# Kernel tuning notes

Measured on AMD Instinct MI355X. Metric: run time of the kernel, lower is better.

## Reference

```python
import jax, jax.numpy as jnp
import numpy as np

B, QL, ML = 8, 128, 1024
QS, KS, H = 512, 512, 256


def setup_inputs() -> dict:
    key = jax.random.key(0)
    ks = jax.random.split(key, 10)
    query = jax.random.normal(ks[0], (B, QL, QS), dtype=jnp.float32)
    memory = jax.random.normal(ks[1], (B, ML, KS), dtype=jnp.float32)
    mask = jax.random.bernoulli(ks[2], 0.1, (B, ML))
    mask = mask.at[:, 0].set(False)  # ensure at least one valid position per row
    s_q = 1.0 / np.sqrt(QS)
    s_k = 1.0 / np.sqrt(KS)
    s_h = 1.0 / np.sqrt(H)
    Wq = jax.random.uniform(ks[3], (H, QS), jnp.float32, -s_q, s_q)
    bq = jax.random.uniform(ks[4], (H,), jnp.float32, -s_q, s_q)
    Wk = jax.random.uniform(ks[5], (H, KS), jnp.float32, -s_k, s_k)
    bk = jax.random.uniform(ks[6], (H,), jnp.float32, -s_k, s_k)
    wl = jax.random.uniform(ks[7], (H,), jnp.float32, -s_h, s_h)
    bl = jax.random.uniform(ks[8], (), jnp.float32, -s_h, s_h)
    return {"query": query, "memory": memory, "mask": mask,
            "Wq": Wq, "bq": bq, "Wk": Wk, "bk": bk, "wl": wl, "bl": bl}


def reference(query, memory, mask, Wq, bq, Wk, bk, wl, bl):
    # q: [B, QL, H], k: [B, ML, H]
    q = jnp.einsum('bqs,hs->bqh', query, Wq) + bq
    k = jnp.einsum('bms,hs->bmh', memory, Wk) + bk
    # additive score: tanh(q + k) projected to scalar  -> [B, QL, ML]
    z = jnp.tanh(q[:, :, None, :] + k[:, None, :, :])  # [B, QL, ML, H]
    logits = jnp.einsum('bqmh,h->bqm', z, wl) + bl
    logits = jnp.where(mask[:, None, :], jnp.float32(-1e18), logits)
    weights = jax.nn.softmax(logits, axis=-1)  # BottleSoftmax over mem_len
    attns = jnp.einsum('bqm,bms->bqs', weights, memory)
    return attns, weights
```

## Files before the change

### kernel.cpp

```cpp
#include <hip/hip_runtime.h>

#define B_  8
#define QL_ 128
#define ML_ 1024
#define KS_ 512
#define H_  256

#define QP_OFF 0
#define KP_OFF 262144
#define MASK_OFF 2359296
#define WH_OFF 2361344
#define WL_OFF 2492416
#define MT_H_OFF 2623488
#define MT_L_OFF 4720640
#define WB_H_OFF 6817792
#define WB_L_OFF 7342080
#define XH_OFF 7866368
#define XL_OFF 10225664
#define WLP_OFF 12584960

typedef __attribute__((ext_vector_type(8))) short bfrag;
typedef __attribute__((ext_vector_type(4))) float f4acc;
typedef __attribute__((ext_vector_type(2))) float f2;

__device__ __forceinline__ void split1(float v, unsigned& h, unsigned& lo) {
    unsigned u  = __float_as_uint(v);
    unsigned hb = u & 0xFFFF0000u;
    float    lf = v - __uint_as_float(hb);
    unsigned ul = __float_as_uint(lf);
    unsigned lr = ul + 0x7FFFu + ((ul >> 16) & 1u);
    h  = u >> 16;
    lo = lr >> 16;
}

__device__ __forceinline__ void split4(const float4& a, unsigned& h01, unsigned& h23,
                                       unsigned& l01, unsigned& l23) {
    unsigned h[4], l[4];
    split1(a.x, h[0], l[0]); split1(a.y, h[1], l[1]);
    split1(a.z, h[2], l[2]); split1(a.w, h[3], l[3]);
    h01 = h[0] | (h[1] << 16); h23 = h[2] | (h[3] << 16);
    l01 = l[0] | (l[1] << 16); l23 = l[2] | (l[3] << 16);
}

__global__ __launch_bounds__(256) void prep_kernel(
    const float* __restrict__ query, const float* __restrict__ memory,
    const float* __restrict__ Wq, const float* __restrict__ Wk,
    const float* __restrict__ wl,
    unsigned short* __restrict__ Whi, unsigned short* __restrict__ Wlo,
    unsigned short* __restrict__ Xhi, unsigned short* __restrict__ Xlo,
    unsigned short* __restrict__ MThi, unsigned short* __restrict__ MTlo,
    const unsigned char* __restrict__ mraw, unsigned char* __restrict__ mout,
    float* __restrict__ wlp) {
    const int bid = blockIdx.x;
    const int t = threadIdx.x;

    if (bid == 2240) {
        wlp[(t & ~7) | (((t & 3) << 1) | ((t >> 2) & 1))] = wl[t];
        __shared__ int s_not01, s_not0f;
        const unsigned int* w = (const unsigned int*)mraw;
        if (t == 0) { s_not01 = 0; s_not0f = 0; }
        __syncthreads();
        int not01 = 0, not0f = 0;
        for (int i = t; i < 2048; i += 256) {
            unsigned int v = w[i];
            if (v != 0u && v != 1u) not01 = 1;
            if (v != 0u && v != 0x3F800000u) not0f = 1;
        }
        if (not01) atomicOr(&s_not01, 1);
        if (not0f) atomicOr(&s_not0f, 1);
        __syncthreads();
        int wordTyped = (!s_not01) || (!s_not0f);
        for (int i = t; i < B_ * ML_; i += 256) {
            unsigned char mv;
            if (wordTyped) mv = (w[i] != 0u) ? 1 : 0;
            else           mv = mraw[i] ? 1 : 0;
            mout[i] = mv;
        }
        return;
    }

    if (bid >= 1216) {
        const int idx = bid - 1216;
        const int b  = idx >> 7;
        const int r  = idx & 127;
        const int mt = r >> 3;
        const int st = r & 7;
        __shared__ float T[64][68];

        const int i  = t >> 2, jb = (t & 3) << 4;
        const float* mp = memory + ((size_t)(b * ML_ + mt * 64 + i)) * KS_ + st * 64 + jb;
#pragma unroll
        for (int q = 0; q < 4; ++q)
            *(float4*)(&T[i][jb + q * 4]) = *(const float4*)(mp + q * 4);
        __syncthreads();

        const int s = t >> 2, mb = (t & 3) << 4;
        unsigned hh[16], ll[16];
#pragma unroll
        for (int e = 0; e < 16; ++e) split1(T[mb + e][s], hh[e], ll[e]);
        unsigned hp[8], lp[8];
#pragma unroll
        for (int e = 0; e < 8; ++e) {
            hp[e] = hh[2 * e] | (hh[2 * e + 1] << 16);
            lp[e] = ll[2 * e] | (ll[2 * e + 1] << 16);
        }
        const size_t doff = ((size_t)(b * KS_ + st * 64 + s)) * ML_ + mt * 64 + mb;
        *(uint4*)(MThi + doff)     = make_uint4(hp[0], hp[1], hp[2], hp[3]);
        *(uint4*)(MThi + doff + 8) = make_uint4(hp[4], hp[5], hp[6], hp[7]);
        *(uint4*)(MTlo + doff)     = make_uint4(lp[0], lp[1], lp[2], lp[3]);
        *(uint4*)(MTlo + doff + 8) = make_uint4(lp[4], lp[5], lp[6], lp[7]);
        return;
    }

    const float* src; unsigned short *dh, *dl; size_t soff, doff;
    if (bid < 64) {
        src = (bid < 32) ? Wq : Wk;
        soff = (size_t)(bid & 31) * 4096;
        doff = ((bid < 32) ? 0 : 131072) + soff;
        dh = Whi; dl = Wlo;
    } else if (bid < 192) {
        src = query;  soff = (size_t)(bid - 64) * 4096;  doff = soff;
        dh = Xhi; dl = Xlo;
    } else {
        src = memory; soff = (size_t)(bid - 192) * 4096; doff = 524288 + soff;
        dh = Xhi; dl = Xlo;
    }
    soff += (size_t)t * 16; doff += (size_t)t * 16;

    unsigned hw[8], lw[8];
#pragma unroll
    for (int i = 0; i < 4; ++i) {
        float4 v = *(const float4*)(src + soff + i * 4);
        split4(v, hw[i * 2], hw[i * 2 + 1], lw[i * 2], lw[i * 2 + 1]);
    }
    *(uint4*)(dh + doff)     = make_uint4(hw[0], hw[1], hw[2], hw[3]);
    *(uint4*)(dh + doff + 8) = make_uint4(hw[4], hw[5], hw[6], hw[7]);
    *(uint4*)(dl + doff)     = make_uint4(lw[0], lw[1], lw[2], lw[3]);
    *(uint4*)(dl + doff + 8) = make_uint4(lw[4], lw[5], lw[6], lw[7]);
}

__global__ __launch_bounds__(256) void proj_kernel(
    const unsigned short* __restrict__ Xhi, const unsigned short* __restrict__ Xlo,
    const unsigned short* __restrict__ Whi, const unsigned short* __restrict__ Wlo,
    const float* __restrict__ bq, const float* __restrict__ bk,
    float* __restrict__ Eq, float* __restrict__ Ek) {
    const int bid = blockIdx.x;
    const int t = threadIdx.x;
    const int wk = (bid & 7) * 144 + (bid >> 3);
    const int nt = wk & 3;
    const int mt = wk >> 2;

    const bool isQ = (mt < 32);
    const int arow0 = mt * 32;
    const int orow0 = isQ ? arow0 : arow0 - 1024;
    const float* bias = isQ ? bq : bk;
    float* out = isQ ? Eq : Ek;
    const int wrb = (isQ ? 0 : 256) + nt * 64;

    const int w  = t >> 6;
    const int wm = w >> 1, wn = w & 1;
    const int l  = t & 63;
    const int lr = l & 15, lk = l >> 4;

    __shared__ unsigned short As[2][2][32][64];
    __shared__ unsigned short Bs[2][2][64][64];

    const int pa   = t >> 7;
    const int slot = t & 127;
    const int arow = slot >> 2, ao = slot & 3;
    const int brow = slot >> 1, bo0 = (slot & 1) * 4;
    const unsigned short* asrc = (pa ? Xlo : Xhi) + (size_t)(arow0 + arow) * 512 + ao * 8;
    const unsigned short* bsrc = (pa ? Wlo : Whi) + (size_t)(wrb + brow) * 512 + bo0 * 8;
    const int awd0 = (ao ^ (arow & 7)) * 8;
    const int awd1 = ((ao + 4) ^ (arow & 7)) * 8;
    int bwd[4];
#pragma unroll
    for (int i = 0; i < 4; ++i) bwd[i] = ((bo0 + i) ^ (brow & 7)) * 8;

    f4acc acc[2];
    acc[0] = (f4acc){0.f, 0.f, 0.f, 0.f};
    acc[1] = (f4acc){0.f, 0.f, 0.f, 0.f};

    uint4 g0a0, g0a1, g0b0, g0b1, g0b2, g0b3;
    uint4 g1a0, g1a1, g1b0, g1b1, g1b2, g1b3;

#define LOADG(G, c) do {                                                  \
    G##a0 = *(const uint4*)(asrc + (size_t)(c) * 64);                     \
    G##a1 = *(const uint4*)(asrc + (size_t)(c) * 64 + 32);                \
    G##b0 = *(const uint4*)(bsrc + (size_t)(c) * 64);                     \
    G##b1 = *(const uint4*)(bsrc + (size_t)(c) * 64 + 8);                 \
    G##b2 = *(const uint4*)(bsrc + (size_t)(c) * 64 + 16);                \
    G##b3 = *(const uint4*)(bsrc + (size_t)(c) * 64 + 24); } while (0)

#define WRITEB(P, G) do {                                                 \
    *(uint4*)(&As[P][pa][arow][awd0])  = G##a0;                           \
    *(uint4*)(&As[P][pa][arow][awd1])  = G##a1;                           \
    *(uint4*)(&Bs[P][pa][brow][bwd[0]]) = G##b0;                          \
    *(uint4*)(&Bs[P][pa][brow][bwd[1]]) = G##b1;                          \
    *(uint4*)(&Bs[P][pa][brow][bwd[2]]) = G##b2;                          \
    *(uint4*)(&Bs[P][pa][brow][bwd[3]]) = G##b3; } while (0)

#define COMPUTE(P) do {                                                   \
    _Pragma("unroll")                                                     \
    for (int ks = 0; ks < 2; ++ks) {                                      \
        const int ra = wm * 16 + lr;                                      \
        const int koA = ((ks * 4 + lk) ^ (ra & 7)) * 8;                   \
        bfrag ah = *(const bfrag*)&As[P][0][ra][koA];                     \
        bfrag al = *(const bfrag*)&As[P][1][ra][koA];                     \
        _Pragma("unroll")                                                 \
        for (int ni = 0; ni < 2; ++ni) {                                  \
            const int rb = wn * 32 + ni * 16 + lr;                        \
            const int koB = ((ks * 4 + lk) ^ (rb & 7)) * 8;               \
            bfrag bh = *(const bfrag*)&Bs[P][0][rb][koB];                 \
            bfrag bl = *(const bfrag*)&Bs[P][1][rb][koB];                 \
            acc[ni] = __builtin_amdgcn_mfma_f32_16x16x32_bf16(            \
                ah, bh, acc[ni], 0, 0, 0);                                \
            acc[ni] = __builtin_amdgcn_mfma_f32_16x16x32_bf16(            \
                ah, bl, acc[ni], 0, 0, 0);                                \
            acc[ni] = __builtin_amdgcn_mfma_f32_16x16x32_bf16(            \
                al, bh, acc[ni], 0, 0, 0);                                \
        }                                                                 \
    } } while (0)

    LOADG(g0, 0);
    WRITEB(0, g0);
    LOADG(g1, 1);
    __syncthreads();

#pragma unroll
    for (int c = 0; c < 8; ++c) {
        if (c + 1 < 8) {
            if ((c + 1) & 1) WRITEB(1, g1); else WRITEB(0, g0);
        }
        if (c + 2 < 8) {
            if (c & 1) LOADG(g1, c + 2); else LOADG(g0, c + 2);
        }
        COMPUTE(c & 1);
        __syncthreads();
    }
#undef LOADG
#undef WRITEB
#undef COMPUTE

    const float SC = 2.885390081777926815f;
#pragma unroll
    for (int ni = 0; ni < 2; ++ni) {
        const int col = nt * 64 + wn * 32 + ni * 16 + lr;
        const int colp = (col & ~7) | (((col & 3) << 1) | ((col >> 2) & 1));
        const float bc = bias[col];
#pragma unroll
        for (int rr = 0; rr < 4; ++rr) {
            const int row = orow0 + wm * 16 + lk * 4 + rr;
            out[(size_t)row * 256 + colp] =
                __builtin_amdgcn_exp2f(SC * (acc[ni][rr] + bc));
        }
    }
}

__device__ __forceinline__ f2 qterm8(const float4 k4a, const float4 k4b,
                                     const float4 q4a, const float4 q4b,
                                     const float4 w4a, const float4 w4b,
                                     f2 acc) {
    f2 kp0 = {k4a.x, k4a.y}, kp1 = {k4a.z, k4a.w};
    f2 kp2 = {k4b.x, k4b.y}, kp3 = {k4b.z, k4b.w};
    f2 qp0 = {q4a.x, q4a.y}, qp1 = {q4a.z, q4a.w};
    f2 qp2 = {q4b.x, q4b.y}, qp3 = {q4b.z, q4b.w};
    f2 wp0 = {w4a.x, w4a.y}, wp1 = {w4a.z, w4a.w};
    f2 wp2 = {w4b.x, w4b.y}, wp3 = {w4b.z, w4b.w};
    const f2 one2 = {1.0f, 1.0f};
    f2 pp0 = __builtin_elementwise_fma(kp0, qp0, one2);
    f2 pp1 = __builtin_elementwise_fma(kp1, qp1, one2);
    f2 pp2 = __builtin_elementwise_fma(kp2, qp2, one2);
    f2 pp3 = __builtin_elementwise_fma(kp3, qp3, one2);
    f2 p01 = pp0 * pp1, p23 = pp2 * pp3;
    f2 n01 = __builtin_elementwise_fma(wp1, pp0, wp0 * pp1);
    f2 n23 = __builtin_elementwise_fma(wp3, pp2, wp2 * pp3);
    f2 Nm  = __builtin_elementwise_fma(n23, p01, n01 * p23);
    f2 P   = p01 * p23;
    f2 r   = {__builtin_amdgcn_rcpf(P.x), __builtin_amdgcn_rcpf(P.y)};
    return __builtin_elementwise_fma(Nm, r, acc);
}

__global__ __launch_bounds__(256) void logits_kernel(
    const float* __restrict__ Eq, const float* __restrict__ Ek,
    const float* __restrict__ wlp, float* __restrict__ sr) {
    const int bid = blockIdx.x;
    const int b  = bid & 7;
    const int r2 = bid >> 3;
    const int mt = r2 & 7;
    const int qt = r2 >> 3;
    const int tid = threadIdx.x;
    const int m  = tid & 127;
    const int qh = __builtin_amdgcn_readfirstlane(tid >> 7);

    __shared__ float kq[2][4][128][4];

    const float* qpb = Eq + ((size_t)(b * QL_ + qt * 8 + qh * 4)) * H_;
    const float* kpb = Ek + ((size_t)(b * ML_ + mt * 128)) * H_;

    const int srow = tid & 127;
    const int sq2  = tid >> 7;
    const float* kst = kpb + (size_t)srow * H_ + 8 * sq2;

    float4 a0 = *(const float4*)(kst);
    float4 a1 = *(const float4*)(kst + 4);
    *(float4*)(&kq[0][2 * sq2 + 0][srow][0]) = a0;
    *(float4*)(&kq[0][2 * sq2 + 1][srow][0]) = a1;
    a0 = *(const float4*)(kst + 16);
    a1 = *(const float4*)(kst + 20);
    __syncthreads();

    f2 accp[4];
#pragma unroll
    for (int j2 = 0; j2 < 4; ++j2) accp[j2] = (f2){0.f, 0.f};

    for (int c = 0; c < 16; ++c) {
        const int cb = c & 1;
        if (c < 15) {
            *(float4*)(&kq[cb ^ 1][2 * sq2 + 0][srow][0]) = a0;
            *(float4*)(&kq[cb ^ 1][2 * sq2 + 1][srow][0]) = a1;
            if (c < 14) {
                a0 = *(const float4*)(kst + (c + 2) * 16);
                a1 = *(const float4*)(kst + (c + 2) * 16 + 4);
            }
        }
        const int h0 = c * 16;
#pragma unroll
        for (int pg = 0; pg < 2; ++pg) {
            float4 k4a = *(const float4*)(&kq[cb][2 * pg + 0][m][0]);
            float4 k4b = *(const float4*)(&kq[cb][2 * pg + 1][m][0]);
            float4 w4a = *(const float4*)(wlp + h0 + pg * 8);
            float4 w4b = *(const float4*)(wlp + h0 + pg * 8 + 4);
#pragma unroll
            for (int j2 = 0; j2 < 4; ++j2) {
                float4 q4a = *(const float4*)(qpb + (size_t)j2 * H_ + h0 + pg * 8);
                float4 q4b = *(const float4*)(qpb + (size_t)j2 * H_ + h0 + pg * 8 + 4);
                accp[j2] = qterm8(k4a, k4b, q4a, q4b, w4a, w4b, accp[j2]);
            }
        }
        __syncthreads();
    }
#pragma unroll
    for (int j2 = 0; j2 < 4; ++j2)
        sr[((size_t)(b * QL_ + qt * 8 + qh * 4 + j2)) * ML_ + mt * 128 + m] =
            accp[j2].x + accp[j2].y;
}

__global__ __launch_bounds__(256) void softmax_kernel(
    float* __restrict__ wrow_io, const unsigned char* __restrict__ mv,
    unsigned short* __restrict__ Wbhi, unsigned short* __restrict__ Wblo) {
    const int row = blockIdx.x;
    const int b = row >> 7;
    const int tid = threadIdx.x;
    float* srow = wrow_io + (size_t)row * ML_;
    const unsigned char* mrow = mv + b * ML_;
    __shared__ float red[4];

    float4 s4 = *(const float4*)(srow + tid * 4);
    uchar4 m4 = *(const uchar4*)(mrow + tid * 4);
    float l[4];
    l[0] = m4.x ? -1e18f : -2.0f * s4.x;
    l[1] = m4.y ? -1e18f : -2.0f * s4.y;
    l[2] = m4.z ? -1e18f : -2.0f * s4.z;
    l[3] = m4.w ? -1e18f : -2.0f * s4.w;

    float mx = fmaxf(fmaxf(l[0], l[1]), fmaxf(l[2], l[3]));
#pragma unroll
    for (int off = 32; off >= 1; off >>= 1)
        mx = fmaxf(mx, __shfl_xor(mx, off));
    if ((tid & 63) == 0) red[tid >> 6] = mx;
    __syncthreads();
    mx = fmaxf(fmaxf(red[0], red[1]), fmaxf(red[2], red[3]));
    __syncthreads();

    const float L2E = 1.44269504088896340736f;
    float e[4], s = 0.f;
#pragma unroll
    for (int i = 0; i < 4; ++i) {
        e[i] = __builtin_amdgcn_exp2f((l[i] - mx) * L2E);
        s += e[i];
    }
#pragma unroll
    for (int off = 32; off >= 1; off >>= 1)
        s += __shfl_xor(s, off);
    if ((tid & 63) == 0) red[tid >> 6] = s;
    __syncthreads();
    s = (red[0] + red[1]) + (red[2] + red[3]);
    float inv = __builtin_amdgcn_rcpf(s);
    float4 o = make_float4(e[0] * inv, e[1] * inv, e[2] * inv, e[3] * inv);
    *(float4*)(srow + tid * 4) = o;

    unsigned h01, h23, l01, l23;
    split4(o, h01, h23, l01, l23);
    *(uint2*)(Wbhi + (size_t)row * ML_ + tid * 4) = make_uint2(h01, h23);
    *(uint2*)(Wblo + (size_t)row * ML_ + tid * 4) = make_uint2(l01, l23);
}

__global__ __launch_bounds__(256) void attn_out_kernel(
    const unsigned short* __restrict__ Wbhi, const unsigned short* __restrict__ Wblo,
    const unsigned short* __restrict__ MThi, const unsigned short* __restrict__ MTlo,
    float* __restrict__ out) {
    const int bid = blockIdx.x;
    const int b  = bid & 7;
    const int r  = bid >> 3;
    const int mt = r & 7;
    const int nt = r >> 3;
    const int t = threadIdx.x;
    const int w  = t >> 6;
    const int l  = t & 63;
    const int lr = l & 15, lk = l >> 4;

    __shared__ unsigned short As[2][16][2][64];
    __shared__ unsigned short Bs[2][64][2][64];

    const int pa  = t >> 7;
    const int ar  = (t >> 3) & 15;
    const int acq = t & 7;
    const unsigned short* asrc = (pa ? Wblo : Wbhi)
        + ((size_t)(b * QL_ + mt * 16 + ar)) * ML_ + acq * 8;
    const int aws = (acq ^ (ar & 7)) * 8;

    const int pb  = t >> 7;
    const int br  = (t & 127) >> 1;
    const int bq0 = (t & 1) * 4;
    const unsigned short* bsrc = (pb ? MTlo : MThi)
        + ((size_t)(b * KS_ + nt * 64 + br)) * ML_ + bq0 * 8;
    int bws[4];
#pragma unroll
    for (int i2 = 0; i2 < 4; ++i2) bws[i2] = ((bq0 + i2) ^ (br & 7)) * 8;

    f4acc acc = (f4acc){0.f, 0.f, 0.f, 0.f};

    uint4 g0a, g0b0, g0b1, g0b2, g0b3;
    uint4 g1a, g1b0, g1b1, g1b2, g1b3;

#define LOADG(G, c) do {                                                  \
    G##a  = *(const uint4*)(asrc + (size_t)(c) * 64);                     \
    G##b0 = *(const uint4*)(bsrc + (size_t)(c) * 64);                     \
    G##b1 = *(const uint4*)(bsrc + (size_t)(c) * 64 + 8);                 \
    G##b2 = *(const uint4*)(bsrc + (size_t)(c) * 64 + 16);                \
    G##b3 = *(const uint4*)(bsrc + (size_t)(c) * 64 + 24); } while (0)

#define WRITEB(P, G) do {                                                 \
    *(uint4*)(&As[P][ar][pa][aws])    = G##a;                             \
    *(uint4*)(&Bs[P][br][pb][bws[0]]) = G##b0;                            \
    *(uint4*)(&Bs[P][br][pb][bws[1]]) = G##b1;                            \
    *(uint4*)(&Bs[P][br][pb][bws[2]]) = G##b2;                            \
    *(uint4*)(&Bs[P][br][pb][bws[3]]) = G##b3; } while (0)

#define COMPUTE(P) do {                                                   \
    _Pragma("unroll")                                                     \
    for (int ks = 0; ks < 2; ++ks) {                                      \
        const int k8 = (ks * 4 + lk) ^ (lr & 7);                          \
        bfrag ah = *(const bfrag*)&As[P][lr][0][k8 * 8];                  \
        bfrag al = *(const bfrag*)&As[P][lr][1][k8 * 8];                  \
        bfrag bh = *(const bfrag*)&Bs[P][w * 16 + lr][0][k8 * 8];         \
        bfrag bl = *(const bfrag*)&Bs[P][w * 16 + lr][1][k8 * 8];         \
        acc = __builtin_amdgcn_mfma_f32_16x16x32_bf16(ah, bh, acc, 0,0,0);\
        acc = __builtin_amdgcn_mfma_f32_16x16x32_bf16(ah, bl, acc, 0,0,0);\
        acc = __builtin_amdgcn_mfma_f32_16x16x32_bf16(al, bh, acc, 0,0,0);\
    } } while (0)

    LOADG(g0, 0);
    WRITEB(0, g0);
    LOADG(g1, 1);
    __syncthreads();

#pragma unroll
    for (int c = 0; c < 16; ++c) {
        if (c + 1 < 16) {
            if ((c + 1) & 1) WRITEB(1, g1); else WRITEB(0, g0);
        }
        if (c + 2 < 16) {
            if (c & 1) LOADG(g1, c + 2); else LOADG(g0, c + 2);
        }
        COMPUTE(c & 1);
        __syncthreads();
    }
#undef LOADG
#undef WRITEB
#undef COMPUTE

    const int col = nt * 64 + w * 16 + lr;
#pragma unroll
    for (int rr = 0; rr < 4; ++rr) {
        const int row = mt * 16 + lk * 4 + rr;
        out[((size_t)(b * QL_ + row)) * KS_ + col] = acc[rr];
    }
}

extern "C" void kernel_launch(void* const* d_in, const int* in_sizes, int n_in,
                              void* d_out, int out_size, void* d_ws, size_t ws_size,
                              hipStream_t stream) {
    const float* query  = (const float*)d_in[0];
    const float* memory = (const float*)d_in[1];
    const unsigned char* mask = (const unsigned char*)d_in[2];
    const float* Wq = (const float*)d_in[3];
    const float* bq = (const float*)d_in[4];
    const float* Wk = (const float*)d_in[5];
    const float* bk = (const float*)d_in[6];
    const float* wl = (const float*)d_in[7];

    float* ws = (float*)d_ws;
    float* Eq = ws + QP_OFF;
    float* Ek = ws + KP_OFF;
    unsigned char* mcan = (unsigned char*)(ws + MASK_OFF);
    unsigned short* Whi  = (unsigned short*)(ws + WH_OFF);
    unsigned short* Wlo  = (unsigned short*)(ws + WL_OFF);
    unsigned short* MThi = (unsigned short*)(ws + MT_H_OFF);
    unsigned short* MTlo = (unsigned short*)(ws + MT_L_OFF);
    unsigned short* Wbhi = (unsigned short*)(ws + WB_H_OFF);
    unsigned short* Wblo = (unsigned short*)(ws + WB_L_OFF);
    unsigned short* Xhi  = (unsigned short*)(ws + XH_OFF);
    unsigned short* Xlo  = (unsigned short*)(ws + XL_OFF);
    float* wlp = ws + WLP_OFF;

    float* attns = (float*)d_out;
    float* wout  = (float*)d_out + B_ * QL_ * KS_;

    prep_kernel<<<dim3(2241), dim3(256), 0, stream>>>(query, memory, Wq, Wk, wl,
                                                      Whi, Wlo, Xhi, Xlo,
                                                      MThi, MTlo, mask, mcan, wlp);
    proj_kernel<<<dim3(1152), dim3(256), 0, stream>>>(Xhi, Xlo, Whi, Wlo,
                                                      bq, bk, Eq, Ek);
    logits_kernel<<<dim3(1024), dim3(256), 0, stream>>>(Eq, Ek, wlp, wout);
    softmax_kernel<<<dim3(B_ * QL_), dim3(256), 0, stream>>>(wout, mcan, Wbhi, Wblo);
    attn_out_kernel<<<dim3(512), dim3(256), 0, stream>>>(Wbhi, Wblo, MThi, MTlo, attns);
}
```

Baseline: 156.9 us.

## Move memory transpose-split into softmax launch and retile logits kernel

Result: no change. 158.5 us (+1.0%).

```diff
diff --git a/kernel.cpp b/kernel.cpp
--- a/kernel.cpp
+++ b/kernel.cpp
@@ -48,13 +48,12 @@
     const float* __restrict__ wl,
     unsigned short* __restrict__ Whi, unsigned short* __restrict__ Wlo,
     unsigned short* __restrict__ Xhi, unsigned short* __restrict__ Xlo,
-    unsigned short* __restrict__ MThi, unsigned short* __restrict__ MTlo,
     const unsigned char* __restrict__ mraw, unsigned char* __restrict__ mout,
     float* __restrict__ wlp) {
     const int bid = blockIdx.x;
     const int t = threadIdx.x;
 
-    if (bid == 2240) {
+    if (bid == 1216) {
         wlp[(t & ~7) | (((t & 3) << 1) | ((t >> 2) & 1))] = wl[t];
         __shared__ int s_not01, s_not0f;
         const unsigned int* w = (const unsigned int*)mraw;
@@ -76,39 +75,6 @@
             else           mv = mraw[i] ? 1 : 0;
             mout[i] = mv;
         }
-        return;
-    }
-
-    if (bid >= 1216) {
-        const int idx = bid - 1216;
-        const int b  = idx >> 7;
-        const int r  = idx & 127;
-        const int mt = r >> 3;
-        const int st = r & 7;
-        __shared__ float T[64][68];
-
-        const int i  = t >> 2, jb = (t & 3) << 4;
-        const float* mp = memory + ((size_t)(b * ML_ + mt * 64 + i)) * KS_ + st * 64 + jb;
-#pragma unroll
-        for (int q = 0; q < 4; ++q)
-            *(float4*)(&T[i][jb + q * 4]) = *(const float4*)(mp + q * 4);
-        __syncthreads();
-
-        const int s = t >> 2, mb = (t & 3) << 4;
-        unsigned hh[16], ll[16];
-#pragma unroll
-        for (int e = 0; e < 16; ++e) split1(T[mb + e][s], hh[e], ll[e]);
-        unsigned hp[8], lp[8];
-#pragma unroll
-        for (int e = 0; e < 8; ++e) {
-            hp[e] = hh[2 * e] | (hh[2 * e + 1] << 16);
-            lp[e] = ll[2 * e] | (ll[2 * e + 1] << 16);
-        }
-        const size_t doff = ((size_t)(b * KS_ + st * 64 + s)) * ML_ + mt * 64 + mb;
-        *(uint4*)(MThi + doff)     = make_uint4(hp[0], hp[1], hp[2], hp[3]);
-        *(uint4*)(MThi + doff + 8) = make_uint4(hp[4], hp[5], hp[6], hp[7]);
-        *(uint4*)(MTlo + doff)     = make_uint4(lp[0], lp[1], lp[2], lp[3]);
-        *(uint4*)(MTlo + doff + 8) = make_uint4(lp[4], lp[5], lp[6], lp[7]);
         return;
     }
 
@@ -287,71 +253,107 @@
     const int bid = blockIdx.x;
     const int b  = bid & 7;
     const int r2 = bid >> 3;
-    const int mt = r2 & 7;
-    const int qt = r2 >> 3;
+    const int mt = r2 & 15;
+    const int qt = r2 >> 4;
     const int tid = threadIdx.x;
-    const int m  = tid & 127;
-    const int qh = __builtin_amdgcn_readfirstlane(tid >> 7);
-
-    __shared__ float kq[2][4][128][4];
-
-    const float* qpb = Eq + ((size_t)(b * QL_ + qt * 8 + qh * 4)) * H_;
-    const float* kpb = Ek + ((size_t)(b * ML_ + mt * 128)) * H_;
-
-    const int srow = tid & 127;
-    const int sq2  = tid >> 7;
-    const float* kst = kpb + (size_t)srow * H_ + 8 * sq2;
+    const int m  = tid & 63;
+    const int qh = __builtin_amdgcn_readfirstlane(tid >> 6);
+
+    __shared__ float kq[2][8][64][4];
+
+    const float* q0 = Eq + ((size_t)(b * QL_ + qt * 8 + qh * 2)) * H_;
+    const float* q1 = q0 + H_;
+    const float* kpb = Ek + ((size_t)(b * ML_ + mt * 64)) * H_;
+
+    const int srow = tid & 63;
+    const int sq   = tid >> 6;
+    const float* kst = kpb + (size_t)srow * H_ + 8 * sq;
 
     float4 a0 = *(const float4*)(kst);
     float4 a1 = *(const float4*)(kst + 4);
-    *(float4*)(&kq[0][2 * sq2 + 0][srow][0]) = a0;
-    *(float4*)(&kq[0][2 * sq2 + 1][srow][0]) = a1;
-    a0 = *(const float4*)(kst + 16);
-    a1 = *(const float4*)(kst + 20);
+    *(float4*)(&kq[0][2 * sq + 0][srow][0]) = a0;
+    *(float4*)(&kq[0][2 * sq + 1][srow][0]) = a1;
+    a0 = *(const float4*)(kst + 32);
+    a1 = *(const float4*)(kst + 36);
     __syncthreads();
 
-    f2 accp[4];
-#pragma unroll
-    for (int j2 = 0; j2 < 4; ++j2) accp[j2] = (f2){0.f, 0.f};
-
-    for (int c = 0; c < 16; ++c) {
+    f2 accp[2];
+    accp[0] = (f2){0.f, 0.f};
+    accp[1] = (f2){0.f, 0.f};
+
+    for (int c = 0; c < 8; ++c) {
         const int cb = c & 1;
-        if (c < 15) {
-            *(float4*)(&kq[cb ^ 1][2 * sq2 + 0][srow][0]) = a0;
-            *(float4*)(&kq[cb ^ 1][2 * sq2 + 1][srow][0]) = a1;
-            if (c < 14) {
-                a0 = *(const float4*)(kst + (c + 2) * 16);
-                a1 = *(const float4*)(kst + (c + 2) * 16 + 4);
+        if (c < 7) {
+            *(float4*)(&kq[cb ^ 1][2 * sq + 0][srow][0]) = a0;
+            *(float4*)(&kq[cb ^ 1][2 * sq + 1][srow][0]) = a1;
+            if (c < 6) {
+                a0 = *(const float4*)(kst + (c + 2) * 32);
+                a1 = *(const float4*)(kst + (c + 2) * 32 + 4);
             }
         }
-        const int h0 = c * 16;
-#pragma unroll
-        for (int pg = 0; pg < 2; ++pg) {
+        const int h0 = c * 32;
+#pragma unroll
+        for (int pg = 0; pg < 4; ++pg) {
             float4 k4a = *(const float4*)(&kq[cb][2 * pg + 0][m][0]);
             float4 k4b = *(const float4*)(&kq[cb][2 * pg + 1][m][0]);
             float4 w4a = *(const float4*)(wlp + h0 + pg * 8);
             float4 w4b = *(const float4*)(wlp + h0 + pg * 8 + 4);
-#pragma unroll
-            for (int j2 = 0; j2 < 4; ++j2) {
-                float4 q4a = *(const float4*)(qpb + (size_t)j2 * H_ + h0 + pg * 8);
-                float4 q4b = *(const float4*)(qpb + (size_t)j2 * H_ + h0 + pg * 8 + 4);
-                accp[j2] = qterm8(k4a, k4b, q4a, q4b, w4a, w4b, accp[j2]);
-            }
+            float4 q4a = *(const float4*)(q0 + h0 + pg * 8);
+            float4 q4b = *(const float4*)(q0 + h0 + pg * 8 + 4);
+            accp[0] = qterm8(k4a, k4b, q4a, q4b, w4a, w4b, accp[0]);
+            q4a = *(const float4*)(q1 + h0 + pg * 8);
+            q4b = *(const float4*)(q1 + h0 + pg * 8 + 4);
+            accp[1] = qterm8(k4a, k4b, q4a, q4b, w4a, w4b, accp[1]);
         }
         __syncthreads();
     }
-#pragma unroll
-    for (int j2 = 0; j2 < 4; ++j2)
-        sr[((size_t)(b * QL_ + qt * 8 + qh * 4 + j2)) * ML_ + mt * 128 + m] =
-            accp[j2].x + accp[j2].y;
+    const size_t ro = ((size_t)(b * QL_ + qt * 8 + qh * 2)) * ML_ + mt * 64 + m;
+    sr[ro]       = accp[0].x + accp[0].y;
+    sr[ro + ML_] = accp[1].x + accp[1].y;
 }
 
 __global__ __launch_bounds__(256) void softmax_kernel(
     float* __restrict__ wrow_io, const unsigned char* __restrict__ mv,
-    unsigned short* __restrict__ Wbhi, unsigned short* __restrict__ Wblo) {
+    unsigned short* __restrict__ Wbhi, unsigned short* __restrict__ Wblo,
+    const float* __restrict__ memory,
+    unsigned short* __restrict__ MThi, unsigned short* __restrict__ MTlo) {
+    const int tid = threadIdx.x;
+
+    if (blockIdx.x >= 1024) {
+        const int idx = blockIdx.x - 1024;
+        const int b  = idx >> 7;
+        const int r  = idx & 127;
+        const int mt = r >> 3;
+        const int st = r & 7;
+        __shared__ float T[64][68];
+
+        const int i  = tid >> 2, jb = (tid & 3) << 4;
+        const float* mp = memory + ((size_t)(b * ML_ + mt * 64 + i)) * KS_ + st * 64 + jb;
+#pragma unroll
+        for (int q = 0; q < 4; ++q)
+            *(float4*)(&T[i][jb + q * 4]) = *(const float4*)(mp + q * 4);
+        __syncthreads();
+
+        const int s = tid >> 2, mb = (tid & 3) << 4;
+        unsigned hh[16], ll[16];
+#pragma unroll
+        for (int e = 0; e < 16; ++e) split1(T[mb + e][s], hh[e], ll[e]);
+        unsigned hp[8], lp[8];
+#pragma unroll
+        for (int e = 0; e < 8; ++e) {
+            hp[e] = hh[2 * e] | (hh[2 * e + 1] << 16);
+            lp[e] = ll[2 * e] | (ll[2 * e + 1] << 16);
+        }
+        const size_t doff = ((size_t)(b * KS_ + st * 64 + s)) * ML_ + mt * 64 + mb;
+        *(uint4*)(MThi + doff)     = make_uint4(hp[0], hp[1], hp[2], hp[3]);
+        *(uint4*)(MThi + doff + 8) = make_uint4(hp[4], hp[5], hp[6], hp[7]);
+        *(uint4*)(MTlo + doff)     = make_uint4(lp[0], lp[1], lp[2], lp[3]);
+        *(uint4*)(MTlo + doff + 8) = make_uint4(lp[4], lp[5], lp[6], lp[7]);
+        return;
+    }
+
     const int row = blockIdx.x;
     const int b = row >> 7;
-    const int tid = threadIdx.x;
     float* srow = wrow_io + (size_t)row * ML_;
     const unsigned char* mrow = mv + b * ML_;
     __shared__ float red[4];
@@ -518,12 +520,12 @@
     float* attns = (float*)d_out;
     float* wout  = (float*)d_out + B_ * QL_ * KS_;
 
-    prep_kernel<<<dim3(2241), dim3(256), 0, stream>>>(query, memory, Wq, Wk, wl,
-                                                      Whi, Wlo, Xhi, Xlo,
-                                                      MThi, MTlo, mask, mcan, wlp);
+    prep_kernel<<<dim3(1217), dim3(256), 0, stream>>>(query, memory, Wq, Wk, wl,
+                                                      Whi, Wlo, Xhi, Xlo, mask, mcan, wlp);
     proj_kernel<<<dim3(1152), dim3(256), 0, stream>>>(Xhi, Xlo, Whi, Wlo,
                                                       bq, bk, Eq, Ek);
-    logits_kernel<<<dim3(1024), dim3(256), 0, stream>>>(Eq, Ek, wlp, wout);
-    softmax_kernel<<<dim3(B_ * QL_), dim3(256), 0, stream>>>(wout, mcan, Wbhi, Wblo);
+    logits_kernel<<<dim3(2048), dim3(256), 0, stream>>>(Eq, Ek, wlp, wout);
+    softmax_kernel<<<dim3(2048), dim3(256), 0, stream>>>(wout, mcan, Wbhi, Wblo,
+                                                         memory, MThi, MTlo);
     attn_out_kernel<<<dim3(512), dim3(256), 0, stream>>>(Wbhi, Wblo, MThi, MTlo, attns);
 }
```
